# Optimization experiments

Measured on AMD Instinct MI355X. Metric: run time of the kernel, lower is better.

The kernel has to match this reference:

```python
import jax, jax.numpy as jnp
import numpy as np

EPS = 1e-4
GRID_RES = 0.01
L = 2
ATOL = 0.01
RTOL = 1e-5


def compute_lub(f_v, edges):
    # f_v: [V,2] vertex filtration values; edges: [E,2] int vertex indices
    e_x = jnp.max(f_v[:, 0][edges], axis=1)  # [E]
    e_y = jnp.max(f_v[:, 1][edges], axis=1)  # [E]
    f_e = jnp.stack([e_x, e_y], axis=1) + EPS  # [E,2]
    return jnp.concatenate([f_v, f_e], axis=0)  # [V+E, 2] = [S,2]


def grad_matrices(filtration, bar, sample_pts):
    # filtration: [S,2], bar: [P,R], sample_pts: [P,2]
    # Vectorized version of the per-point Python loops in moveSimplices.forward.
    S = filtration.shape[0]
    P = sample_pts.shape[0]
    fx, fy = filtration[:, 0], filtration[:, 1]          # [S]
    px, py = sample_pts[:, 0], sample_pts[:, 1]          # [P]
    fsum = fx + fy                                        # [S]
    psum = px + py                                        # [P]
    shift = jnp.arange(-L, L + 1, dtype=filtration.dtype)  # [5]
    tol_x = ATOL + RTOL * jnp.abs(fx)                     # torch.isclose tolerance
    tol_y = ATOL + RTOL * jnp.abs(fy)
    below = fsum[None, :] < psum[:, None]                 # [P,S]
    above = fsum[None, :] > psum[:, None]

    Gs, Gcs = [], []
    for r in range(bar.shape[1]):  # small fixed rank loop (R=3)
        s = bar[:, r] + GRID_RES                          # [P]
        line_x = shift[None, :] * s[:, None] + px[:, None]  # [P,5]
        line_y = shift[None, :] * s[:, None] + py[:, None]
        last_x, last_y = line_x[:, -1], line_y[:, -1]      # [P] (shift=+L endpoint)
        # isclose over shifts, reduced with any() (duplicate scatter writes are idempotent)
        hit_x = (jnp.abs(line_x[:, None, :] - fx[None, :, None]) <= tol_x[None, :, None]).any(-1)  # [P,S]
        hit_y = (jnp.abs(line_y[:, None, :] - fy[None, :, None]) <= tol_y[None, :, None]).any(-1)
        lx = hit_x & (fy[None, :] <= last_y[:, None]) & below
        ux = hit_x & (fy[None, :] <= last_y[:, None]) & above
        ly = hit_y & (fx[None, :] <= last_x[:, None]) & below
        uy = hit_y & (fx[None, :] <= last_x[:, None]) & above
        vx = ux.astype(filtration.dtype) - lx.astype(filtration.dtype)  # +1 upper, -1 lower (exclusive)
        vy = uy.astype(filtration.dtype) - ly.astype(filtration.dtype)
        G = jnp.stack([vx, vy], axis=-1).reshape(P, 2 * S)  # interleave x,y columns
        cx = jnp.where(ux.any(1), -1.0, jnp.where(lx.any(1), 1.0, 0.0)).astype(filtration.dtype)
        cy = jnp.where(uy.any(1), -1.0, jnp.where(ly.any(1), 1.0, 0.0)).astype(filtration.dtype)
        Gc = jnp.stack([cx, cy], axis=-1)                  # [P,2]
        Gs.append(G)
        Gcs.append(Gc)
    return jnp.stack(Gs), jnp.stack(Gcs)  # [R,P,2S], [R,P,2]


def setup_inputs() -> dict:
    key = jax.random.key(0)
    k1, k2, k3, k4, k5 = jax.random.split(key, 5)
    V, E, P, R = 1200, 4800, 2500, 3
    f_v = jax.random.uniform(k1, (V, 2), dtype=jnp.float32)
    edges = jax.random.randint(k2, (E, 2), 0, V, dtype=jnp.int64)
    bars0 = jax.random.uniform(k3, (P, R), dtype=jnp.float32)
    bars1 = jax.random.uniform(k4, (P, R), dtype=jnp.float32)
    sample_pts = jax.random.uniform(k5, (P, 2), dtype=jnp.float32)
    return {"f_v": f_v, "edges": edges, "bars0": bars0, "bars1": bars1, "sample_pts": sample_pts}


def reference(f_v, edges, bars0, bars1, sample_pts):
    filtration = compute_lub(f_v, edges)
    G0, Gc0 = grad_matrices(filtration, bars0, sample_pts)
    G1, Gc1 = grad_matrices(filtration, bars1, sample_pts)
    # moveSimplices.forward returns the bars unchanged; the grad matrices are the
    # saved side outputs (ctx.grad_matrices_*) and the kernel-heavy computation.
    return (bars0, bars1, G0, G1, Gc0, Gc1)
```

## Files before the change

### kernel.cpp

```cpp
#include <hip/hip_runtime.h>

#define EPS_F      1e-4f
#define GRID_RES_F 0.01f
#define ATOL_F     0.01f
#define RTOL_F     1e-5f

static constexpr int V = 1200;
static constexpr int E = 4800;
static constexpr int S = V + E;
static constexpr int P = 2500;
static constexpr int R = 3;

static constexpr size_t G0_BASE  = 15000ull;
static constexpr size_t G_ELEMS  = (size_t)R * P * 2 * S;
static constexpr size_t GC0_BASE = G0_BASE + 2 * G_ELEMS;

__global__ void build_filt_kernel(const float* __restrict__ f_v,
                                  const int*   __restrict__ edges,
                                  float4*      __restrict__ filt) {
    int j = blockIdx.x * blockDim.x + threadIdx.x;
    if (j >= S) return;
    float fx, fy;
    if (j < V) {
        fx = f_v[2 * j];
        fy = f_v[2 * j + 1];
    } else {
        int e = j - V;
        int a = edges[2 * e];
        int b = edges[2 * e + 1];
        fx = __fadd_rn(fmaxf(f_v[2 * a],     f_v[2 * b]),     EPS_F);
        fy = __fadd_rn(fmaxf(f_v[2 * a + 1], f_v[2 * b + 1]), EPS_F);
    }
    float tolx = __fadd_rn(ATOL_F, __fmul_rn(RTOL_F, fabsf(fx)));
    float toly = __fadd_rn(ATOL_F, __fmul_rn(RTOL_F, fabsf(fy)));
    filt[j] = make_float4(fx, fy, tolx, toly);
}

__device__ __forceinline__ float mindist(const float* l, float f) {
    float a = fabsf(__fsub_rn(l[0], f));
    float b = fabsf(__fsub_rn(l[1], f));
    float c = fabsf(__fsub_rn(l[2], f));
    float d = fabsf(__fsub_rn(l[3], f));
    float e = fabsf(__fsub_rn(l[4], f));
    return fminf(fminf(fminf(a, b), fminf(c, d)), e);
}

__device__ __forceinline__ void cell(const float4& f, float psum,
                                     const float* lxs, const float* lys,
                                     float& vx, float& vy,
                                     int& aux, int& alx, int& auy, int& aly) {
    float fsum = __fadd_rn(f.x, f.y);
    bool ab = fsum > psum, be = fsum < psum;
    float sg = ab ? 1.0f : (be ? -1.0f : 0.0f);
    bool cx = (mindist(lxs, f.x) <= f.z) && (f.y <= lys[4]);
    bool cy = (mindist(lys, f.y) <= f.w) && (f.x <= lxs[4]);
    vx = cx ? sg : 0.0f;
    vy = cy ? sg : 0.0f;
    aux |= (int)(cx && ab); alx |= (int)(cx && be);
    auy |= (int)(cy && ab); aly |= (int)(cy && be);
}

__global__ __launch_bounds__(256) void grad_kernel(
        const float4* __restrict__ filt,
        const float*  __restrict__ bars0,
        const float*  __restrict__ bars1,
        const float*  __restrict__ sample_pts,
        float*        __restrict__ d_out) {
    const int p = blockIdx.x;
    const int r = blockIdx.y;
    const int b = blockIdx.z;

    const float* bar = (b == 0) ? bars0 : bars1;
    const float px = sample_pts[2 * p];
    const float py = sample_pts[2 * p + 1];
    const float psum = __fadd_rn(px, py);
    const float s  = __fadd_rn(bar[p * R + r], GRID_RES_F);
    const float s2 = __fmul_rn(2.0f, s);

    float lxs[5], lys[5];
    lxs[0] = __fadd_rn(-s2, px); lxs[1] = __fadd_rn(-s, px); lxs[2] = px;
    lxs[3] = __fadd_rn( s, px);  lxs[4] = __fadd_rn(s2, px);
    lys[0] = __fadd_rn(-s2, py); lys[1] = __fadd_rn(-s, py); lys[2] = py;
    lys[3] = __fadd_rn( s, py);  lys[4] = __fadd_rn(s2, py);

    float* Grow = d_out + G0_BASE + (size_t)b * G_ELEMS
                        + ((size_t)(r * P + p)) * (2 * S);

    __shared__ int sh_flags[4];
    if (threadIdx.x < 4) sh_flags[threadIdx.x] = 0;
    __syncthreads();

    int aux = 0, alx = 0, auy = 0, aly = 0;

    int j = threadIdx.x * 4;
    float4 a0, a1, a2, a3;
    if (j < S) { a0 = filt[j]; a1 = filt[j+1]; a2 = filt[j+2]; a3 = filt[j+3]; }
    while (j < S) {
        const int jn = j + 1024;
        float4 b0, b1, b2, b3;
        if (jn < S) {
            b0 = filt[jn]; b1 = filt[jn+1]; b2 = filt[jn+2]; b3 = filt[jn+3];
        }
        float4 o0, o1;
        cell(a0, psum, lxs, lys, o0.x, o0.y, aux, alx, auy, aly);
        cell(a1, psum, lxs, lys, o0.z, o0.w, aux, alx, auy, aly);
        cell(a2, psum, lxs, lys, o1.x, o1.y, aux, alx, auy, aly);
        cell(a3, psum, lxs, lys, o1.z, o1.w, aux, alx, auy, aly);
        float4* dst = reinterpret_cast<float4*>(Grow + 2 * j);
        dst[0] = o0;
        dst[1] = o1;
        a0 = b0; a1 = b1; a2 = b2; a3 = b3;
        j = jn;
    }

    if (aux) sh_flags[0] = 1;
    if (alx) sh_flags[1] = 1;
    if (auy) sh_flags[2] = 1;
    if (aly) sh_flags[3] = 1;
    __syncthreads();

    if (threadIdx.x == 0) {
        float cx = sh_flags[0] ? -1.0f : (sh_flags[1] ? 1.0f : 0.0f);
        float cy = sh_flags[2] ? -1.0f : (sh_flags[3] ? 1.0f : 0.0f);
        size_t gc = GC0_BASE + (size_t)b * ((size_t)R * P * 2)
                             + ((size_t)(r * P + p)) * 2;
        d_out[gc]     = cx;
        d_out[gc + 1] = cy;
    }
}

extern "C" void kernel_launch(void* const* d_in, const int* in_sizes, int n_in,
                              void* d_out, int out_size, void* d_ws, size_t ws_size,
                              hipStream_t stream) {
    const float* f_v        = (const float*)d_in[0];
    const int*   edges      = (const int*)d_in[1];
    const float* bars0      = (const float*)d_in[2];
    const float* bars1      = (const float*)d_in[3];
    const float* sample_pts = (const float*)d_in[4];
    float* out = (float*)d_out;

    float4* filt = (float4*)d_ws;

    (void)hipMemcpyAsync(out,         bars0, (size_t)P * R * sizeof(float),
                         hipMemcpyDeviceToDevice, stream);
    (void)hipMemcpyAsync(out + P * R, bars1, (size_t)P * R * sizeof(float),
                         hipMemcpyDeviceToDevice, stream);

    build_filt_kernel<<<(S + 255) / 256, 256, 0, stream>>>(f_v, edges, filt);

    dim3 grid(P, R, 2);
    grad_kernel<<<grid, 256, 0, stream>>>(filt, bars0, bars1, sample_pts, out);
}
```

Measured before the change: 726.1 us.

## Fuse all six rank/bar combos per sample point into one block with nontemporal stores

Each block now handles one sample point for all six (bar set, rank) combinations, so every filtration element it loads is reused six times instead of being reloaded by six separate blocks. Block size goes to 512 threads with two elements per thread, and the flag reductions are packed into per-combo bitmasks. Output rows are written with nontemporal stores because the output is large and never reread. This gives 2500 blocks instead of 15000, which costs parallelism, and six widely separated output streams per block.

```diff
diff --git a/kernel.cpp b/kernel.cpp
--- a/kernel.cpp
+++ b/kernel.cpp
@@ -11,9 +11,13 @@
 static constexpr int P = 2500;
 static constexpr int R = 3;
 
-static constexpr size_t G0_BASE  = 15000ull;
-static constexpr size_t G_ELEMS  = (size_t)R * P * 2 * S;
-static constexpr size_t GC0_BASE = G0_BASE + 2 * G_ELEMS;
+typedef float v4f __attribute__((ext_vector_type(4)));
+
+static constexpr size_t G0_BASE      = 15000ull;
+static constexpr size_t ROW_LEN      = 2ull * S;
+static constexpr size_t COMBO_STRIDE = (size_t)P * ROW_LEN;
+static constexpr size_t G_ELEMS      = (size_t)R * COMBO_STRIDE;
+static constexpr size_t GC0_BASE     = G0_BASE + 2 * G_ELEMS;
 
 __global__ void build_filt_kernel(const float* __restrict__ f_v,
                                   const int*   __restrict__ edges,
@@ -47,7 +51,7 @@
 
 __device__ __forceinline__ void cell(const float4& f, float psum,
                                      const float* lxs, const float* lys,
-                                     float& vx, float& vy,
+                                     float& vx, float& vy, int bit,
                                      int& aux, int& alx, int& auy, int& aly) {
     float fsum = __fadd_rn(f.x, f.y);
     bool ab = fsum > psum, be = fsum < psum;
@@ -56,74 +60,86 @@
     bool cy = (mindist(lys, f.y) <= f.w) && (f.x <= lxs[4]);
     vx = cx ? sg : 0.0f;
     vy = cy ? sg : 0.0f;
-    aux |= (int)(cx && ab); alx |= (int)(cx && be);
-    auy |= (int)(cy && ab); aly |= (int)(cy && be);
+    if (cx && ab) aux |= bit;
+    if (cx && be) alx |= bit;
+    if (cy && ab) auy |= bit;
+    if (cy && be) aly |= bit;
 }
 
-__global__ __launch_bounds__(256) void grad_kernel(
+__global__ __launch_bounds__(512) void grad_kernel(
         const float4* __restrict__ filt,
         const float*  __restrict__ bars0,
         const float*  __restrict__ bars1,
         const float*  __restrict__ sample_pts,
         float*        __restrict__ d_out) {
     const int p = blockIdx.x;
-    const int r = blockIdx.y;
-    const int b = blockIdx.z;
 
-    const float* bar = (b == 0) ? bars0 : bars1;
     const float px = sample_pts[2 * p];
     const float py = sample_pts[2 * p + 1];
     const float psum = __fadd_rn(px, py);
-    const float s  = __fadd_rn(bar[p * R + r], GRID_RES_F);
-    const float s2 = __fmul_rn(2.0f, s);
 
-    float lxs[5], lys[5];
-    lxs[0] = __fadd_rn(-s2, px); lxs[1] = __fadd_rn(-s, px); lxs[2] = px;
-    lxs[3] = __fadd_rn( s, px);  lxs[4] = __fadd_rn(s2, px);
-    lys[0] = __fadd_rn(-s2, py); lys[1] = __fadd_rn(-s, py); lys[2] = py;
-    lys[3] = __fadd_rn( s, py);  lys[4] = __fadd_rn(s2, py);
+    float sv[6], s2v[6];
+#pragma unroll
+    for (int c = 0; c < 6; ++c) {
+        const float* bar = (c < 3) ? bars0 : bars1;
+        const int r = (c < 3) ? c : c - 3;
+        const float s = __fadd_rn(bar[p * R + r], GRID_RES_F);
+        sv[c]  = s;
+        s2v[c] = __fmul_rn(2.0f, s);
+    }
 
-    float* Grow = d_out + G0_BASE + (size_t)b * G_ELEMS
-                        + ((size_t)(r * P + p)) * (2 * S);
+    float* gbase = d_out + G0_BASE + (size_t)p * ROW_LEN;
 
-    __shared__ int sh_flags[4];
-    if (threadIdx.x < 4) sh_flags[threadIdx.x] = 0;
+    __shared__ int shf[24];
+    if (threadIdx.x < 24) shf[threadIdx.x] = 0;
     __syncthreads();
 
     int aux = 0, alx = 0, auy = 0, aly = 0;
 
-    int j = threadIdx.x * 4;
-    float4 a0, a1, a2, a3;
-    if (j < S) { a0 = filt[j]; a1 = filt[j+1]; a2 = filt[j+2]; a3 = filt[j+3]; }
+    int j = threadIdx.x * 2;
+    float4 a0, a1;
+    if (j < S) { a0 = filt[j]; a1 = filt[j + 1]; }
     while (j < S) {
         const int jn = j + 1024;
-        float4 b0, b1, b2, b3;
+        float4 b0, b1;
         if (jn < S) {
-            b0 = filt[jn]; b1 = filt[jn+1]; b2 = filt[jn+2]; b3 = filt[jn+3];
+            b0 = filt[jn]; b1 = filt[jn + 1];
         }
-        float4 o0, o1;
-        cell(a0, psum, lxs, lys, o0.x, o0.y, aux, alx, auy, aly);
-        cell(a1, psum, lxs, lys, o0.z, o0.w, aux, alx, auy, aly);
-        cell(a2, psum, lxs, lys, o1.x, o1.y, aux, alx, auy, aly);
-        cell(a3, psum, lxs, lys, o1.z, o1.w, aux, alx, auy, aly);
-        float4* dst = reinterpret_cast<float4*>(Grow + 2 * j);
-        dst[0] = o0;
-        dst[1] = o1;
-        a0 = b0; a1 = b1; a2 = b2; a3 = b3;
+#pragma unroll
+        for (int c = 0; c < 6; ++c) {
+            const float s = sv[c], s2 = s2v[c];
+            float lxs[5], lys[5];
+            lxs[0] = __fadd_rn(-s2, px); lxs[1] = __fadd_rn(-s, px); lxs[2] = px;
+            lxs[3] = __fadd_rn( s, px);  lxs[4] = __fadd_rn( s2, px);
+            lys[0] = __fadd_rn(-s2, py); lys[1] = __fadd_rn(-s, py); lys[2] = py;
+            lys[3] = __fadd_rn( s, py);  lys[4] = __fadd_rn( s2, py);
+            const int bit = 1 << c;
+            v4f o;
+            float ox, oy, oz, ow;
+            cell(a0, psum, lxs, lys, ox, oy, bit, aux, alx, auy, aly);
+            cell(a1, psum, lxs, lys, oz, ow, bit, aux, alx, auy, aly);
+            o.x = ox; o.y = oy; o.z = oz; o.w = ow;
+            __builtin_nontemporal_store(o,
+                reinterpret_cast<v4f*>(gbase + c * COMBO_STRIDE + 2 * (size_t)j));
+        }
+        a0 = b0; a1 = b1;
         j = jn;
     }
 
-    if (aux) sh_flags[0] = 1;
-    if (alx) sh_flags[1] = 1;
-    if (auy) sh_flags[2] = 1;
-    if (aly) sh_flags[3] = 1;
+#pragma unroll
+    for (int c = 0; c < 6; ++c) {
+        if (aux & (1 << c)) shf[c]      = 1;
+        if (alx & (1 << c)) shf[6 + c]  = 1;
+        if (auy & (1 << c)) shf[12 + c] = 1;
+        if (aly & (1 << c)) shf[18 + c] = 1;
+    }
     __syncthreads();
 
-    if (threadIdx.x == 0) {
-        float cx = sh_flags[0] ? -1.0f : (sh_flags[1] ? 1.0f : 0.0f);
-        float cy = sh_flags[2] ? -1.0f : (sh_flags[3] ? 1.0f : 0.0f);
-        size_t gc = GC0_BASE + (size_t)b * ((size_t)R * P * 2)
-                             + ((size_t)(r * P + p)) * 2;
+    if (threadIdx.x < 6) {
+        const int c = threadIdx.x;
+        float cx = shf[c]      ? -1.0f : (shf[6 + c]  ? 1.0f : 0.0f);
+        float cy = shf[12 + c] ? -1.0f : (shf[18 + c] ? 1.0f : 0.0f);
+        size_t gc = GC0_BASE + (size_t)c * ((size_t)P * 2) + (size_t)p * 2;
         d_out[gc]     = cx;
         d_out[gc + 1] = cy;
     }
@@ -148,6 +164,5 @@
 
     build_filt_kernel<<<(S + 255) / 256, 256, 0, stream>>>(f_v, edges, filt);
 
-    dim3 grid(P, R, 2);
-    grad_kernel<<<grid, 256, 0, stream>>>(filt, bars0, bars1, sample_pts, out);
+    grad_kernel<<<dim3(P), 512, 0, stream>>>(filt, bars0, bars1, sample_pts, out);
 }
```

Measured after the change: 781.1 us. 7.6% more time.
